# Optimization experiments

Measured on AMD Instinct MI355X. Metric: run time of the kernel, lower is better.

The kernel has to match this reference:

```python
import jax, jax.numpy as jnp
import numpy as np

P = 256         # ids_per_batch
K = 16          # imgs_per_id
D = 2048        # feature_dim
MARGIN = 10.0
EPS = 1e-12


def setup_inputs() -> dict:
    key = jax.random.key(0)
    features = jax.random.normal(key, (P * K, D), dtype=jnp.float32)
    # ordered batch: label i repeated K times, matching targets[0::imgs_per_id] slicing
    targets = jnp.repeat(jnp.arange(P, dtype=jnp.int64), K)
    return {"features": features, "targets": targets}


def reference(features, targets):
    # ordered path: batch == P*K, labels grouped -> reshape replaces the per-class python loop
    f = features.reshape(P, K, D)               # [P, K, D]
    centers = f.mean(axis=1)                    # [P, D] per-class mean

    # intra: euclidean dist from each center to its own K features, max per class
    intra_d2 = jnp.sum((f - centers[:, None, :]) ** 2, axis=-1)     # [P, K]
    intra_max = jnp.max(jnp.sqrt(jnp.clip(intra_d2, EPS, None)), axis=1)  # [P]

    # inter: pairwise center distances, min over other centers
    cc = jnp.sum(centers ** 2, axis=1)                              # [P]
    cd2 = cc[:, None] + cc[None, :] - 2.0 * (centers @ centers.T)   # [P, P]
    cd = jnp.sqrt(jnp.clip(cd2, EPS, None))
    cd = jnp.where(jnp.eye(P, dtype=bool), jnp.inf, cd)             # exclude self
    inter_min = jnp.min(cd, axis=1)                                 # [P]

    cluster_loss = jnp.mean(jax.nn.relu(intra_max - inter_min + MARGIN))
    return cluster_loss, intra_max, inter_min
```

## Files before the change

kernel.cpp:

```cpp
#include <hip/hip_runtime.h>
#include <math.h>

#define NP 256
#define NK 16
#define ND 2048
#define MARGIN 10.0f
#define EPSV 1e-12f
#define NBLK_B 64

typedef short bf16x8 __attribute__((ext_vector_type(8)));
typedef float f32x4 __attribute__((ext_vector_type(4)));

static __device__ __forceinline__ unsigned short f2bf(float f) {
  unsigned u = __float_as_uint(f);
  return (unsigned short)((u + 0x7fffu + ((u >> 16) & 1u)) >> 16);
}

__global__ __launch_bounds__(512) void k_center_intra(
    const float* __restrict__ F, unsigned short* __restrict__ Cb,
    float* __restrict__ cc, int* __restrict__ ticket,
    float* __restrict__ out) {
  const int p = blockIdx.x;
  const int t = threadIdx.x;
  const int wave = t >> 6, lane = t & 63;
  const int d = t * 4;

  float4 x[NK];
#pragma unroll
  for (int k = 0; k < NK; ++k)
    x[k] = *reinterpret_cast<const float4*>(&F[((size_t)(p * NK + k)) * ND + d]);
#pragma unroll
  for (int k = 0; k < NK; ++k)
    asm volatile("" : "+v"(x[k].x), "+v"(x[k].y), "+v"(x[k].z), "+v"(x[k].w));

  float4 c;
  c.x = c.y = c.z = c.w = 0.f;
#pragma unroll
  for (int k = 0; k < NK; ++k) {
    c.x += x[k].x; c.y += x[k].y; c.z += x[k].z; c.w += x[k].w;
  }
  const float inv = 1.0f / 16.0f;
  c.x *= inv; c.y *= inv; c.z *= inv; c.w *= inv;

  ushort4 cb;
  cb.x = f2bf(c.x); cb.y = f2bf(c.y); cb.z = f2bf(c.z); cb.w = f2bf(c.w);
  *reinterpret_cast<ushort4*>(&Cb[(size_t)p * ND + d]) = cb;

  float ccp = c.x * c.x + c.y * c.y + c.z * c.z + c.w * c.w;

  float acc[NK];
#pragma unroll
  for (int k = 0; k < NK; ++k) {
    float dx = x[k].x - c.x, dy = x[k].y - c.y;
    float dz = x[k].z - c.z, dw = x[k].w - c.w;
    acc[k] = dx * dx + dy * dy + dz * dz + dw * dw;
  }

#pragma unroll
  for (int k = 0; k < NK; ++k) {
    float v = acc[k];
#pragma unroll
    for (int m = 32; m > 0; m >>= 1) v += __shfl_xor(v, m);
    acc[k] = v;
  }
  {
    float v = ccp;
#pragma unroll
    for (int m = 32; m > 0; m >>= 1) v += __shfl_xor(v, m);
    ccp = v;
  }

  __shared__ float red[8][NK + 1];
  if (lane == 0) {
#pragma unroll
    for (int k = 0; k < NK; ++k) red[wave][k] = acc[k];
    red[wave][NK] = ccp;
  }
  __syncthreads();
  if (t == 0) {
    float m = 0.f;
#pragma unroll
    for (int k = 0; k < NK; ++k) {
      float s = 0.f;
#pragma unroll
      for (int w = 0; w < 8; ++w) s += red[w][k];
      m = fmaxf(m, sqrtf(fmaxf(s, EPSV)));
    }
    out[1 + p] = m;
    float s = 0.f;
#pragma unroll
    for (int w = 0; w < 8; ++w) s += red[w][NK];
    cc[p] = s;
    reinterpret_cast<int*>(out)[1 + NP + p] = 0x7f800000;
    if (p == 0) atomicExch(ticket, 0);
  }
}

__global__ __launch_bounds__(256) void k_pair_loss(
    const unsigned short* __restrict__ Cb, const float* __restrict__ cc,
    int* __restrict__ ticket, float* __restrict__ out) {
  const int t = threadIdx.x;
  const int wave = t >> 6, lane = t & 63;
  const int tile = blockIdx.x * 4 + wave;
  const int pi = tile >> 4, qi = tile & 15;
  const int lr = lane & 15;
  const int kg = (lane >> 4) * 8;

  const unsigned short* ap = &Cb[(size_t)(pi * 16 + lr) * ND + kg];
  const unsigned short* bp = &Cb[(size_t)(qi * 16 + lr) * ND + kg];

  f32x4 a0 = {0.f, 0.f, 0.f, 0.f}, a1 = a0, a2 = a0, a3 = a0;
#pragma unroll
  for (int i = 0; i < 16; ++i) {
    bf16x8 av0 = *reinterpret_cast<const bf16x8*>(ap + i * 128);
    bf16x8 bv0 = *reinterpret_cast<const bf16x8*>(bp + i * 128);
    bf16x8 av1 = *reinterpret_cast<const bf16x8*>(ap + i * 128 + 32);
    bf16x8 bv1 = *reinterpret_cast<const bf16x8*>(bp + i * 128 + 32);
    bf16x8 av2 = *reinterpret_cast<const bf16x8*>(ap + i * 128 + 64);
    bf16x8 bv2 = *reinterpret_cast<const bf16x8*>(bp + i * 128 + 64);
    bf16x8 av3 = *reinterpret_cast<const bf16x8*>(ap + i * 128 + 96);
    bf16x8 bv3 = *reinterpret_cast<const bf16x8*>(bp + i * 128 + 96);
    a0 = __builtin_amdgcn_mfma_f32_16x16x32_bf16(av0, bv0, a0, 0, 0, 0);
    a1 = __builtin_amdgcn_mfma_f32_16x16x32_bf16(av1, bv1, a1, 0, 0, 0);
    a2 = __builtin_amdgcn_mfma_f32_16x16x32_bf16(av2, bv2, a2, 0, 0, 0);
    a3 = __builtin_amdgcn_mfma_f32_16x16x32_bf16(av3, bv3, a3, 0, 0, 0);
  }
  f32x4 acc = a0 + a1 + a2 + a3;

  const int rbase = (lane >> 4) * 4;
  const int qg = qi * 16 + lr;
  const float ccq = cc[qg];
  float cdm[4];
#pragma unroll
  for (int r = 0; r < 4; ++r) {
    const int pg = pi * 16 + rbase + r;
    const float cd2 = cc[pg] + ccq - 2.0f * acc[r];
    cdm[r] = (pg == qg) ? INFINITY : sqrtf(fmaxf(cd2, EPSV));
  }
#pragma unroll
  for (int r = 0; r < 4; ++r) {
#pragma unroll
    for (int m = 8; m > 0; m >>= 1) cdm[r] = fminf(cdm[r], __shfl_xor(cdm[r], m));
  }
  if (lr == 0) {
#pragma unroll
    for (int r = 0; r < 4; ++r)
      atomicMin(reinterpret_cast<int*>(out) + 1 + NP + pi * 16 + rbase + r,
                __float_as_int(cdm[r]));
  }

  __syncthreads();
  __threadfence();
  __shared__ int my_ticket;
  if (t == 0) my_ticket = atomicAdd(ticket, 1);
  __syncthreads();
  if (my_ticket == NBLK_B - 1) {
    const float im = out[1 + t];
    const int bits = atomicOr(reinterpret_cast<int*>(out) + 1 + NP + t, 0);
    const float in_ = __int_as_float(bits);
    float v = fmaxf(im - in_ + MARGIN, 0.f);
#pragma unroll
    for (int m = 32; m > 0; m >>= 1) v += __shfl_xor(v, m);
    __shared__ float red[4];
    if (lane == 0) red[wave] = v;
    __syncthreads();
    if (t == 0) out[0] = (red[0] + red[1] + red[2] + red[3]) / (float)NP;
  }
}

extern "C" void kernel_launch(void* const* d_in, const int* in_sizes, int n_in,
                              void* d_out, int out_size, void* d_ws,
                              size_t ws_size, hipStream_t stream) {
  const float* F = (const float*)d_in[0];
  float* out = (float*)d_out;

  unsigned short* Cb = (unsigned short*)d_ws;
  float* cc = (float*)(Cb + (size_t)NP * ND);
  int* ticket = (int*)(cc + NP);

  k_center_intra<<<NP, 512, 0, stream>>>(F, Cb, cc, ticket, out);
  k_pair_loss<<<NBLK_B, 256, 0, stream>>>(Cb, cc, ticket, out);
}
```

Before: 34.41 us.

## Split K across waves in pair kernel and widen center kernel to 1024 threads

The pair-distance kernel now gives each 16x16 tile its own block and splits the 2048-long dot product across four waves, combining the partial sums through shared memory. This gives 256 blocks instead of 64. The center/intra kernel uses 1024 threads with float2 loads, and 17 threads finish the reduction in parallel instead of a single thread. The aim is more parallelism and shorter serial tails, at the cost of extra shared-memory traffic, a block sync, and more atomics and ticket increments.

```diff
diff --git a/kernel.cpp b/kernel.cpp
--- a/kernel.cpp
+++ b/kernel.cpp
@@ -6,7 +6,7 @@
 #define ND 2048
 #define MARGIN 10.0f
 #define EPSV 1e-12f
-#define NBLK_B 64
+#define NBLK_B 256
 
 typedef short bf16x8 __attribute__((ext_vector_type(8)));
 typedef float f32x4 __attribute__((ext_vector_type(4)));
@@ -16,44 +16,41 @@
   return (unsigned short)((u + 0x7fffu + ((u >> 16) & 1u)) >> 16);
 }
 
-__global__ __launch_bounds__(512) void k_center_intra(
+__global__ __launch_bounds__(1024) void k_center_intra(
     const float* __restrict__ F, unsigned short* __restrict__ Cb,
     float* __restrict__ cc, int* __restrict__ ticket,
     float* __restrict__ out) {
   const int p = blockIdx.x;
   const int t = threadIdx.x;
   const int wave = t >> 6, lane = t & 63;
-  const int d = t * 4;
+  const int d = t * 2;
 
-  float4 x[NK];
+  float2 x[NK];
 #pragma unroll
   for (int k = 0; k < NK; ++k)
-    x[k] = *reinterpret_cast<const float4*>(&F[((size_t)(p * NK + k)) * ND + d]);
+    x[k] = *reinterpret_cast<const float2*>(&F[((size_t)(p * NK + k)) * ND + d]);
 #pragma unroll
   for (int k = 0; k < NK; ++k)
-    asm volatile("" : "+v"(x[k].x), "+v"(x[k].y), "+v"(x[k].z), "+v"(x[k].w));
+    asm volatile("" : "+v"(x[k].x), "+v"(x[k].y));
 
-  float4 c;
-  c.x = c.y = c.z = c.w = 0.f;
+  float2 c;
+  c.x = c.y = 0.f;
 #pragma unroll
-  for (int k = 0; k < NK; ++k) {
-    c.x += x[k].x; c.y += x[k].y; c.z += x[k].z; c.w += x[k].w;
-  }
+  for (int k = 0; k < NK; ++k) { c.x += x[k].x; c.y += x[k].y; }
   const float inv = 1.0f / 16.0f;
-  c.x *= inv; c.y *= inv; c.z *= inv; c.w *= inv;
+  c.x *= inv; c.y *= inv;
 
-  ushort4 cb;
-  cb.x = f2bf(c.x); cb.y = f2bf(c.y); cb.z = f2bf(c.z); cb.w = f2bf(c.w);
-  *reinterpret_cast<ushort4*>(&Cb[(size_t)p * ND + d]) = cb;
+  ushort2 cb;
+  cb.x = f2bf(c.x); cb.y = f2bf(c.y);
+  *reinterpret_cast<ushort2*>(&Cb[(size_t)p * ND + d]) = cb;
 
-  float ccp = c.x * c.x + c.y * c.y + c.z * c.z + c.w * c.w;
+  float ccp = c.x * c.x + c.y * c.y;
 
   float acc[NK];
 #pragma unroll
   for (int k = 0; k < NK; ++k) {
     float dx = x[k].x - c.x, dy = x[k].y - c.y;
-    float dz = x[k].z - c.z, dw = x[k].w - c.w;
-    acc[k] = dx * dx + dy * dy + dz * dz + dw * dw;
+    acc[k] = dx * dx + dy * dy;
   }
 
 #pragma unroll
@@ -70,27 +67,27 @@
     ccp = v;
   }
 
-  __shared__ float red[8][NK + 1];
+  __shared__ float red[16][NK + 2];
   if (lane == 0) {
 #pragma unroll
     for (int k = 0; k < NK; ++k) red[wave][k] = acc[k];
     red[wave][NK] = ccp;
   }
   __syncthreads();
-  if (t == 0) {
-    float m = 0.f;
-#pragma unroll
-    for (int k = 0; k < NK; ++k) {
-      float s = 0.f;
-#pragma unroll
-      for (int w = 0; w < 8; ++w) s += red[w][k];
-      m = fmaxf(m, sqrtf(fmaxf(s, EPSV)));
-    }
-    out[1 + p] = m;
+  if (t < NK + 1) {
     float s = 0.f;
 #pragma unroll
-    for (int w = 0; w < 8; ++w) s += red[w][NK];
-    cc[p] = s;
+    for (int w = 0; w < 16; ++w) s += red[w][t];
+    if (t == NK) {
+      cc[p] = s;
+    } else {
+      float v = sqrtf(fmaxf(s, EPSV));
+#pragma unroll
+      for (int m = 8; m > 0; m >>= 1) v = fmaxf(v, __shfl_xor(v, m));
+      if (t == 0) out[1 + p] = v;
+    }
+  }
+  if (t == 0) {
     reinterpret_cast<int*>(out)[1 + NP + p] = 0x7f800000;
     if (p == 0) atomicExch(ticket, 0);
   }
@@ -99,19 +96,19 @@
 __global__ __launch_bounds__(256) void k_pair_loss(
     const unsigned short* __restrict__ Cb, const float* __restrict__ cc,
     int* __restrict__ ticket, float* __restrict__ out) {
+  const int b = blockIdx.x;
   const int t = threadIdx.x;
   const int wave = t >> 6, lane = t & 63;
-  const int tile = blockIdx.x * 4 + wave;
-  const int pi = tile >> 4, qi = tile & 15;
+  const int pi = b >> 4, qi = b & 15;
   const int lr = lane & 15;
   const int kg = (lane >> 4) * 8;
 
-  const unsigned short* ap = &Cb[(size_t)(pi * 16 + lr) * ND + kg];
-  const unsigned short* bp = &Cb[(size_t)(qi * 16 + lr) * ND + kg];
+  const unsigned short* ap = &Cb[(size_t)(pi * 16 + lr) * ND + wave * 512 + kg];
+  const unsigned short* bp = &Cb[(size_t)(qi * 16 + lr) * ND + wave * 512 + kg];
 
   f32x4 a0 = {0.f, 0.f, 0.f, 0.f}, a1 = a0, a2 = a0, a3 = a0;
 #pragma unroll
-  for (int i = 0; i < 16; ++i) {
+  for (int i = 0; i < 4; ++i) {
     bf16x8 av0 = *reinterpret_cast<const bf16x8*>(ap + i * 128);
     bf16x8 bv0 = *reinterpret_cast<const bf16x8*>(bp + i * 128);
     bf16x8 av1 = *reinterpret_cast<const bf16x8*>(ap + i * 128 + 32);
@@ -127,26 +124,22 @@
   }
   f32x4 acc = a0 + a1 + a2 + a3;
 
-  const int rbase = (lane >> 4) * 4;
-  const int qg = qi * 16 + lr;
-  const float ccq = cc[qg];
-  float cdm[4];
+  __shared__ float red2[4][256];
 #pragma unroll
-  for (int r = 0; r < 4; ++r) {
-    const int pg = pi * 16 + rbase + r;
-    const float cd2 = cc[pg] + ccq - 2.0f * acc[r];
-    cdm[r] = (pg == qg) ? INFINITY : sqrtf(fmaxf(cd2, EPSV));
-  }
+  for (int r = 0; r < 4; ++r) red2[wave][lane * 4 + r] = acc[r];
+  __syncthreads();
+
+  {
+    float g = red2[0][t] + red2[1][t] + red2[2][t] + red2[3][t];
+    const int row = ((t >> 6) & 3) * 4 + (t & 3);
+    const int col = (t >> 2) & 15;
+    const int p = pi * 16 + row, q = qi * 16 + col;
+    const float cd2 = cc[p] + cc[q] - 2.0f * g;
+    float cd = (p == q) ? INFINITY : sqrtf(fmaxf(cd2, EPSV));
 #pragma unroll
-  for (int r = 0; r < 4; ++r) {
-#pragma unroll
-    for (int m = 8; m > 0; m >>= 1) cdm[r] = fminf(cdm[r], __shfl_xor(cdm[r], m));
-  }
-  if (lr == 0) {
-#pragma unroll
-    for (int r = 0; r < 4; ++r)
-      atomicMin(reinterpret_cast<int*>(out) + 1 + NP + pi * 16 + rbase + r,
-                __float_as_int(cdm[r]));
+    for (int m = 4; m <= 32; m <<= 1) cd = fminf(cd, __shfl_xor(cd, m));
+    if (col == 0)
+      atomicMin(reinterpret_cast<int*>(out) + 1 + NP + p, __float_as_int(cd));
   }
 
   __syncthreads();
@@ -161,10 +154,10 @@
     float v = fmaxf(im - in_ + MARGIN, 0.f);
 #pragma unroll
     for (int m = 32; m > 0; m >>= 1) v += __shfl_xor(v, m);
-    __shared__ float red[4];
-    if (lane == 0) red[wave] = v;
+    __shared__ float red3[4];
+    if (lane == 0) red3[wave] = v;
     __syncthreads();
-    if (t == 0) out[0] = (red[0] + red[1] + red[2] + red[3]) / (float)NP;
+    if (t == 0) out[0] = (red3[0] + red3[1] + red3[2] + red3[3]) / (float)NP;
   }
 }
 
@@ -178,6 +171,6 @@
   float* cc = (float*)(Cb + (size_t)NP * ND);
   int* ticket = (int*)(cc + NP);
 
-  k_center_intra<<<NP, 512, 0, stream>>>(F, Cb, cc, ticket, out);
+  k_center_intra<<<NP, 1024, 0, stream>>>(F, Cb, cc, ticket, out);
   k_pair_loss<<<NBLK_B, 256, 0, stream>>>(Cb, cc, ticket, out);
 }
```

Result: slower. 35.77 us (+4.0%).
